# Kernel optimization log

Hardware: AMD Instinct MI355X
Metric: run time of the kernel (lower is better)

## Reference

```python
import jax, jax.numpy as jnp
import numpy as np

S = 3072        # total tokens (3 images x 1024 patches)
E = 1280        # n_embed
H = 16          # n_heads
HD = E // H     # head_dim = 80
NSEG = 3


def rotate_half(x):
    x1 = x[..., : x.shape[-1] // 2]
    x2 = x[..., x.shape[-1] // 2 :]
    return jnp.concatenate((-x2, x1), axis=-1)


def setup_inputs() -> dict:
    key = jax.random.key(0)
    ks = jax.random.split(key, 6)
    x = jax.random.normal(ks[0], (S, E), dtype=jnp.float32)
    rotary_pos_emb = jax.random.normal(ks[1], (S, HD // 2), dtype=jnp.float32)
    qkv_w = jax.random.normal(ks[2], (3 * E, E), dtype=jnp.float32) * 0.02
    qkv_b = jax.random.normal(ks[3], (3 * E,), dtype=jnp.float32) * 0.02
    proj_w = jax.random.normal(ks[4], (E, E), dtype=jnp.float32) * 0.02
    proj_b = jax.random.normal(ks[5], (E,), dtype=jnp.float32) * 0.02
    cu_seqlens = (jnp.arange(NSEG + 1, dtype=jnp.int32) * (S // NSEG))  # [0,1024,2048,3072]
    return {"x": x, "rotary_pos_emb": rotary_pos_emb, "qkv_w": qkv_w,
            "qkv_b": qkv_b, "proj_w": proj_w, "proj_b": proj_b,
            "cu_seqlens": cu_seqlens}


def reference(x, rotary_pos_emb, qkv_w, qkv_b, proj_w, proj_b, cu_seqlens):
    seq_len = x.shape[0]
    # qkv projection (torch Linear: x @ W.T + b)
    qkv = (x @ qkv_w.T + qkv_b).reshape(seq_len, 3, H, HD)
    q, k, v = qkv[:, 0], qkv[:, 1], qkv[:, 2]          # each [S, H, HD]

    # inline RoPE: cos/sin repeated over the two halves of head_dim
    cos = jnp.cos(rotary_pos_emb)
    sin = jnp.sin(rotary_pos_emb)
    cos = jnp.concatenate([cos, cos], axis=-1)[:, None, :]  # [S, 1, HD]
    sin = jnp.concatenate([sin, sin], axis=-1)[:, None, :]
    q = q * cos + rotate_half(q) * sin
    k = k * cos + rotate_half(k) * sin

    # block-diagonal segment mask from cu_seqlens
    seg = jnp.searchsorted(cu_seqlens, jnp.arange(seq_len), side="right")  # [S]
    mask = seg[:, None] == seg[None, :]                 # [S, S] bool

    scale = jnp.asarray(1.0 / np.sqrt(HD), dtype=q.dtype)
    scores = jnp.einsum("qhd,khd->hqk", q, k) * scale   # [H, S, S]
    scores = jnp.where(mask[None], scores, jnp.finfo(scores.dtype).min)
    attn = jax.nn.softmax(scores, axis=-1)
    out = jnp.einsum("hqk,khd->qhd", attn, v).reshape(seq_len, E)
    return out @ proj_w.T + proj_b
```

## Files before the change

kernel.cpp:

```cpp
#include <hip/hip_runtime.h>
#include <hip/hip_bf16.h>
#include <math.h>

#define SEQ   3072
#define EMB   1280
#define NHEAD 16
#define HDIM  80
#define QKVN  3840
#define NSEGS 3

typedef __attribute__((ext_vector_type(8))) short bf16x8;
typedef __attribute__((ext_vector_type(4))) short bf16x4;
typedef __attribute__((ext_vector_type(4))) float f32x4;

__device__ __forceinline__ short f2bf(float f) {
    __hip_bfloat16 h = __float2bfloat16(f);
    return *reinterpret_cast<short*>(&h);
}
__device__ __forceinline__ float bf2f(short s) {
    unsigned int u = ((unsigned int)(unsigned short)s) << 16;
    union { unsigned int u; float f; } c; c.u = u;
    return c.f;
}

__device__ __forceinline__ void gload_lds16(const void* g, void* l) {
    __builtin_amdgcn_global_load_lds(
        (const __attribute__((address_space(1))) unsigned int*)g,
        (__attribute__((address_space(3))) unsigned int*)l, 16, 0, 0);
}

__global__ __launch_bounds__(256)
void cvt3_kernel(const float* __restrict__ a, short* __restrict__ oa, int na8,
                 const float* __restrict__ b, short* __restrict__ ob, int nb8,
                 const float* __restrict__ c, short* __restrict__ oc, int nc8)
{
    int j = blockIdx.x * 256 + threadIdx.x;
    const float* src; short* dst;
    if (j < na8) { src = a; dst = oa; }
    else if ((j -= na8) < nb8) { src = b; dst = ob; }
    else { j -= nb8; src = c; dst = oc; }
    float4 x = *reinterpret_cast<const float4*>(&src[j*8]);
    float4 y = *reinterpret_cast<const float4*>(&src[j*8+4]);
    bf16x8 o;
    o[0]=f2bf(x.x); o[1]=f2bf(x.y); o[2]=f2bf(x.z); o[3]=f2bf(x.w);
    o[4]=f2bf(y.x); o[5]=f2bf(y.y); o[6]=f2bf(y.z); o[7]=f2bf(y.w);
    *reinterpret_cast<bf16x8*>(&dst[j*8]) = o;
}

__device__ __forceinline__ void store_val(float v, float* p) { *p = v; }
__device__ __forceinline__ void store_val(float v, short* p) { *p = f2bf(v); }

template<typename OT, bool SWZ>
__global__ __launch_bounds__(256)
void gemm_bf16_nt(const short* __restrict__ A, int lda,
                  const short* __restrict__ B,
                  const float* __restrict__ bias, OT* __restrict__ C,
                  int M, int N, int K)
{
    __shared__ short As[128][32];
    __shared__ short Bs[128][32];

    int bx, by;
    if (SWZ) {
        const int flat = blockIdx.x;
        const int xcd  = flat & 7;
        const int i    = flat >> 3;
        by = xcd * 3 + (i % 3);
        bx = i / 3;
    } else {
        bx = blockIdx.x;
        by = blockIdx.y;
    }

    const int tid = threadIdx.x;
    const int w   = tid >> 6;
    const int l   = tid & 63;
    const int l15 = l & 15;
    const int l4  = l >> 4;
    const int wr  = w >> 1;
    const int wc  = w & 1;
    const int row0 = by * 128;
    const int col0 = bx * 128;

    const int srow = l >> 2;
    const int sk   = (l & 3) * 8;

    f32x4 acc[4][4];
    #pragma unroll
    for (int mi = 0; mi < 4; ++mi)
        #pragma unroll
        for (int ni = 0; ni < 4; ++ni) acc[mi][ni] = (f32x4){0.f,0.f,0.f,0.f};

    for (int k0 = 0; k0 < K; k0 += 32) {
        {
            const int c0 = w, c1 = w + 4;
            gload_lds16(&A[(size_t)(row0 + c0*16 + srow) * lda + k0 + sk], &As[c0*16][0]);
            gload_lds16(&A[(size_t)(row0 + c1*16 + srow) * lda + k0 + sk], &As[c1*16][0]);
            gload_lds16(&B[(size_t)(col0 + c0*16 + srow) * K   + k0 + sk], &Bs[c0*16][0]);
            gload_lds16(&B[(size_t)(col0 + c1*16 + srow) * K   + k0 + sk], &Bs[c1*16][0]);
        }
        __syncthreads();

        bf16x8 af[4], bfr[4];
        #pragma unroll
        for (int mi = 0; mi < 4; ++mi)
            af[mi] = *reinterpret_cast<const bf16x8*>(&As[wr*64 + mi*16 + l15][l4*8]);
        #pragma unroll
        for (int ni = 0; ni < 4; ++ni)
            bfr[ni] = *reinterpret_cast<const bf16x8*>(&Bs[wc*64 + ni*16 + l15][l4*8]);

        #pragma unroll
        for (int mi = 0; mi < 4; ++mi)
            #pragma unroll
            for (int ni = 0; ni < 4; ++ni)
                acc[mi][ni] = __builtin_amdgcn_mfma_f32_16x16x32_bf16(
                    af[mi], bfr[ni], acc[mi][ni], 0, 0, 0);
        __syncthreads();
    }

    #pragma unroll
    for (int ni = 0; ni < 4; ++ni) {
        int col = col0 + wc*64 + ni*16 + l15;
        float bv = bias[col];
        #pragma unroll
        for (int mi = 0; mi < 4; ++mi) {
            #pragma unroll
            for (int r = 0; r < 4; ++r) {
                size_t row = (size_t)(row0 + wr*64 + mi*16 + l4*4 + r);
                store_val(acc[mi][ni][r] + bv, &C[row * (size_t)N + col]);
            }
        }
    }
}

template<typename OT>
__global__ __launch_bounds__(256)
void gemm_bf16_nt64(const short* __restrict__ A, int lda,
                    const short* __restrict__ B,
                    const float* __restrict__ bias, OT* __restrict__ C,
                    int M, int N, int K)
{
    __shared__ short As[128][32];
    __shared__ short Bs[64][32];

    const int tid = threadIdx.x;
    const int w   = tid >> 6;
    const int l   = tid & 63;
    const int l15 = l & 15;
    const int l4  = l >> 4;
    const int wr  = w >> 1;
    const int wc  = w & 1;
    const int row0 = blockIdx.y * 128;
    const int col0 = blockIdx.x * 64;

    const int srow = l >> 2;
    const int sk   = (l & 3) * 8;

    f32x4 acc[4][2];
    #pragma unroll
    for (int mi = 0; mi < 4; ++mi)
        #pragma unroll
        for (int ni = 0; ni < 2; ++ni) acc[mi][ni] = (f32x4){0.f,0.f,0.f,0.f};

    for (int k0 = 0; k0 < K; k0 += 32) {
        {
            const int c0 = w, c1 = w + 4;
            gload_lds16(&A[(size_t)(row0 + c0*16 + srow) * lda + k0 + sk], &As[c0*16][0]);
            gload_lds16(&A[(size_t)(row0 + c1*16 + srow) * lda + k0 + sk], &As[c1*16][0]);
            gload_lds16(&B[(size_t)(col0 + w*16  + srow) * K   + k0 + sk], &Bs[w*16][0]);
        }
        __syncthreads();

        bf16x8 af[4], bfr[2];
        #pragma unroll
        for (int mi = 0; mi < 4; ++mi)
            af[mi] = *reinterpret_cast<const bf16x8*>(&As[wr*64 + mi*16 + l15][l4*8]);
        #pragma unroll
        for (int ni = 0; ni < 2; ++ni)
            bfr[ni] = *reinterpret_cast<const bf16x8*>(&Bs[wc*32 + ni*16 + l15][l4*8]);

        #pragma unroll
        for (int mi = 0; mi < 4; ++mi)
            #pragma unroll
            for (int ni = 0; ni < 2; ++ni)
                acc[mi][ni] = __builtin_amdgcn_mfma_f32_16x16x32_bf16(
                    af[mi], bfr[ni], acc[mi][ni], 0, 0, 0);
        __syncthreads();
    }

    #pragma unroll
    for (int ni = 0; ni < 2; ++ni) {
        int col = col0 + wc*32 + ni*16 + l15;
        float bv = bias[col];
        #pragma unroll
        for (int mi = 0; mi < 4; ++mi) {
            #pragma unroll
            for (int r = 0; r < 4; ++r) {
                size_t row = (size_t)(row0 + wr*64 + mi*16 + l4*4 + r);
                store_val(acc[mi][ni][r] + bv, &C[row * (size_t)N + col]);
            }
        }
    }
}

__global__ __launch_bounds__(256)
void rope_bf16_kernel(short* __restrict__ qkv, const float* __restrict__ rpe)
{
    int idx = blockIdx.x * 256 + threadIdx.x;
    int blk = idx % 5;
    int h   = (idx / 5) % NHEAD;
    int s   = (idx / (5*NHEAD)) % SEQ;
    int t   = idx / (5*NHEAD*SEQ);
    int d0  = blk * 8;

    const float* rp = rpe + s*40 + d0;
    short* p = qkv + (size_t)s*QKVN + t*EMB + h*HDIM + d0;
    bf16x8 v0 = *reinterpret_cast<const bf16x8*>(p);
    bf16x8 v1 = *reinterpret_cast<const bf16x8*>(p + 40);
    bf16x8 o0, o1;
    #pragma unroll
    for (int j = 0; j < 8; ++j) {
        float ang = rp[j];
        float sn = sinf(ang), cs = cosf(ang);
        float a = bf2f(v0[j]), b = bf2f(v1[j]);
        o0[j] = f2bf(a*cs - b*sn);
        o1[j] = f2bf(b*cs + a*sn);
    }
    *reinterpret_cast<bf16x8*>(p)      = o0;
    *reinterpret_cast<bf16x8*>(p + 40) = o1;
}

__global__ __launch_bounds__(256, 4)
void attn_mfma(const short* __restrict__ qkv, const int* __restrict__ cu,
               short* __restrict__ aout)
{
    const int flat = blockIdx.x;
    const int xcd  = flat & 7;
    const int rem  = flat >> 3;
    const int qt   = rem & 15;
    const int shhi = rem >> 4;
    const int sh   = xcd + 8*shhi;
    const int h    = sh / 3;
    const int seg  = sh - 3*h;
    const int s0 = cu[seg], s1 = cu[seg+1];

    const int tid = threadIdx.x;
    const int w   = tid >> 6;
    const int l   = tid & 63;
    const int l15 = l & 15;
    const int l4  = l >> 4;

    __shared__ short Kl[64][128];
    __shared__ short Vt[HDIM][64];

    const int q0 = s0 + qt*64 + w*16;

    bf16x8 bzero;
    #pragma unroll
    for (int j = 0; j < 8; ++j) bzero[j] = 0;

    bf16x8 qf[3];
    {
        const short* qp = qkv + (size_t)(q0 + l15) * QKVN + h*HDIM;
        qf[0] = *reinterpret_cast<const bf16x8*>(qp + l4*8);
        qf[1] = *reinterpret_cast<const bf16x8*>(qp + 32 + l4*8);
        qf[2] = (l4 < 2) ? *reinterpret_cast<const bf16x8*>(qp + 64 + l4*8) : bzero;
    }

    float m = -3.4e38f, lsum = 0.f;
    f32x4 O[5];
    #pragma unroll
    for (int dt = 0; dt < 5; ++dt) O[dt] = (f32x4){0.f,0.f,0.f,0.f};

    int kkey[3], ku[3];
    const short* kptr[3];
    short* klds[3];
    #pragma unroll
    for (int i = 0; i < 3; ++i) {
        int task = tid + i*256;
        kkey[i] = task / 12;
        ku[i]   = task - kkey[i]*12;
        kptr[i] = qkv + (size_t)(s0 + kkey[i])*QKVN + EMB + h*HDIM + ku[i]*8;
        klds[i] = &Kl[kkey[i]][(ku[i] ^ (kkey[i] & 7))*8];
    }

    const int vu  = ((l >> 2) & 3) | ((l >> 5) << 2);
    const int vbs = ((l >> 4) & 1) * 4 + (l & 3);
    const int vd0 = w * 20;
    const short* vp1 = qkv + (size_t)(s0 + l) * QKVN + 2*EMB + h*HDIM + vd0;

    bf16x8 kreg[3];
    bf16x8 vA, vB;
    bf16x4 vC;
    #pragma unroll
    for (int i = 0; i < 3; ++i)
        kreg[i] = (ku[i] < 10) ? *reinterpret_cast<const bf16x8*>(kptr[i]) : bzero;
    vA = *reinterpret_cast<const bf16x8*>(vp1);
    vB = *reinterpret_cast<const bf16x8*>(vp1 + 8);
    vC = *reinterpret_cast<const bf16x4*>(vp1 + 16);

    const float scale2 = 0.1612982054f;
    const int nk = s1 - s0;
    const size_t step = (size_t)64 * QKVN;
    short* vt_flat = &Vt[0][0];

    for (int kc = 0; kc < nk; kc += 64) {
        __syncthreads();

        #pragma unroll
        for (int i = 0; i < 3; ++i)
            *reinterpret_cast<bf16x8*>(klds[i]) = kreg[i];
        #pragma unroll
        for (int e = 0; e < 8; ++e) {
            int d = vd0 + e;
            vt_flat[d*64 + ((vu ^ (d & 7)) & 7)*8 + vbs] = vA[e];
        }
        #pragma unroll
        for (int e = 0; e < 8; ++e) {
            int d = vd0 + 8 + e;
            vt_flat[d*64 + ((vu ^ (d & 7)) & 7)*8 + vbs] = vB[e];
        }
        #pragma unroll
        for (int e = 0; e < 4; ++e) {
            int d = vd0 + 16 + e;
            vt_flat[d*64 + ((vu ^ (d & 7)) & 7)*8 + vbs] = vC[e];
        }

        if (kc + 64 < nk) {
            #pragma unroll
            for (int i = 0; i < 3; ++i) {
                kptr[i] += step;
                if (ku[i] < 10) kreg[i] = *reinterpret_cast<const bf16x8*>(kptr[i]);
            }
            vp1 += step;
            vA = *reinterpret_cast<const bf16x8*>(vp1);
            vB = *reinterpret_cast<const bf16x8*>(vp1 + 8);
            vC = *reinterpret_cast<const bf16x4*>(vp1 + 16);
        }
        __syncthreads();

        f32x4 S[4];
        __builtin_amdgcn_s_setprio(1);
        #pragma unroll
        for (int ct = 0; ct < 4; ++ct) {
            f32x4 acc = (f32x4){0.f,0.f,0.f,0.f};
            int key = ct*16 + l15;
            #pragma unroll
            for (int t = 0; t < 3; ++t) {
                int u = (4*t + l4) ^ (key & 7);
                bf16x8 a = *reinterpret_cast<const bf16x8*>(&Kl[key][u*8]);
                acc = __builtin_amdgcn_mfma_f32_16x16x32_bf16(a, qf[t], acc, 0, 0, 0);
            }
            S[ct] = acc;
        }
        __builtin_amdgcn_s_setprio(0);

        float mxr = -3.4e38f;
        #pragma unroll
        for (int ct = 0; ct < 4; ++ct)
            #pragma unroll
            for (int r = 0; r < 4; ++r) mxr = fmaxf(mxr, S[ct][r]);
        float mx = mxr * scale2;
        mx = fmaxf(mx, __shfl_xor(mx, 16));
        mx = fmaxf(mx, __shfl_xor(mx, 32));
        if (!__all(mx - m <= 8.f)) {
            float mn   = fmaxf(m, mx);
            float corr = exp2f(m - mn);
            lsum *= corr;
            #pragma unroll
            for (int dt = 0; dt < 5; ++dt)
                #pragma unroll
                for (int r = 0; r < 4; ++r) O[dt][r] *= corr;
            m = mn;
        }
        float p[4][4];
        float ps = 0.f;
        #pragma unroll
        for (int ct = 0; ct < 4; ++ct)
            #pragma unroll
            for (int r = 0; r < 4; ++r) {
                float e = exp2f(fmaf(S[ct][r], scale2, -m));
                p[ct][r] = e;
                ps += e;
            }
        ps += __shfl_xor(ps, 16);
        ps += __shfl_xor(ps, 32);
        lsum += ps;

        #pragma unroll
        for (int s2 = 0; s2 < 2; ++s2) {
            bf16x8 pb;
            #pragma unroll
            for (int j = 0; j < 8; ++j)
                pb[j] = f2bf(p[2*s2 + (j>>2)][j & 3]);
            __builtin_amdgcn_s_setprio(1);
            #pragma unroll
            for (int dt = 0; dt < 5; ++dt) {
                int d = dt*16 + l15;
                bf16x8 va = *reinterpret_cast<const bf16x8*>(
                    &vt_flat[d*64 + (((4*s2 + l4) ^ (d & 7)) & 7)*8]);
                O[dt] = __builtin_amdgcn_mfma_f32_16x16x32_bf16(va, pb, O[dt], 0, 0, 0);
            }
            __builtin_amdgcn_s_setprio(0);
        }
    }

    float inv = 1.f / lsum;
    short* orow = aout + (size_t)(q0 + l15) * EMB + h*HDIM;
    #pragma unroll
    for (int dt = 0; dt < 5; ++dt) {
        bf16x4 o4;
        #pragma unroll
        for (int r = 0; r < 4; ++r) o4[r] = f2bf(O[dt][r] * inv);
        *reinterpret_cast<bf16x4*>(&orow[dt*16 + 4*l4]) = o4;
    }
}

extern "C" void kernel_launch(void* const* d_in, const int* in_sizes, int n_in,
                              void* d_out, int out_size, void* d_ws, size_t ws_size,
                              hipStream_t stream)
{
    const float* x      = (const float*)d_in[0];
    const float* rpe    = (const float*)d_in[1];
    const float* qkv_w  = (const float*)d_in[2];
    const float* qkv_b  = (const float*)d_in[3];
    const float* proj_w = (const float*)d_in[4];
    const float* proj_b = (const float*)d_in[5];
    const int*   cu     = (const int*)d_in[6];
    float* out = (float*)d_out;

    short* ws       = (short*)d_ws;
    short* qkv_bf   = ws;
    short* x_bf     = qkv_bf  + (size_t)SEQ * QKVN;
    short* qkvw_bf  = x_bf    + (size_t)SEQ * EMB;
    short* projw_bf = qkvw_bf + (size_t)QKVN * EMB;
    short* attn_bf  = projw_bf+ (size_t)EMB * EMB;

    dim3 blk(256);

    const int na8 = SEQ*EMB/8, nb8 = QKVN*EMB/8, nc8 = EMB*EMB/8;
    cvt3_kernel<<<dim3((na8+nb8+nc8)/256), blk, 0, stream>>>(
        x, x_bf, na8, qkv_w, qkvw_bf, nb8, proj_w, projw_bf, nc8);

    gemm_bf16_nt<short, true><<<dim3((QKVN/128)*(SEQ/128)), blk, 0, stream>>>(
        x_bf, EMB, qkvw_bf, qkv_b, qkv_bf, SEQ, QKVN, EMB);

    rope_bf16_kernel<<<dim3(2*SEQ*NHEAD*5/256), blk, 0, stream>>>(qkv_bf, rpe);

    attn_mfma<<<dim3(16*NSEGS*NHEAD), blk, 0, stream>>>(qkv_bf, cu, attn_bf);

    gemm_bf16_nt64<float><<<dim3(EMB/64, SEQ/128), blk, 0, stream>>>(
        attn_bf, EMB, projw_bf, proj_b, out, SEQ, EMB, EMB);
}
```

Before: 136.2 us.

## Double-buffer LDS tiles in bf16 GEMM kernels to overlap loads with MFMA

Both NT GEMM kernels now use two LDS buffers for A and B tiles, issuing the async global-to-LDS load for the next K-slice before computing on the current one. This cuts barriers per K step from two to one and hides global load latency behind MFMA work. It doubles LDS usage per block, which may reduce occupancy.

```diff
diff --git a/kernel.cpp b/kernel.cpp
--- a/kernel.cpp
+++ b/kernel.cpp
@@ -57,8 +57,8 @@
                   const float* __restrict__ bias, OT* __restrict__ C,
                   int M, int N, int K)
 {
-    __shared__ short As[128][32];
-    __shared__ short Bs[128][32];
+    __shared__ short As0[128][32], Bs0[128][32];
+    __shared__ short As1[128][32], Bs1[128][32];
 
     int bx, by;
     if (SWZ) {
@@ -84,6 +84,7 @@
 
     const int srow = l >> 2;
     const int sk   = (l & 3) * 8;
+    const int c0 = w, c1 = w + 4;
 
     f32x4 acc[4][4];
     #pragma unroll
@@ -91,32 +92,44 @@
         #pragma unroll
         for (int ni = 0; ni < 4; ++ni) acc[mi][ni] = (f32x4){0.f,0.f,0.f,0.f};
 
-    for (int k0 = 0; k0 < K; k0 += 32) {
-        {
-            const int c0 = w, c1 = w + 4;
-            gload_lds16(&A[(size_t)(row0 + c0*16 + srow) * lda + k0 + sk], &As[c0*16][0]);
-            gload_lds16(&A[(size_t)(row0 + c1*16 + srow) * lda + k0 + sk], &As[c1*16][0]);
-            gload_lds16(&B[(size_t)(col0 + c0*16 + srow) * K   + k0 + sk], &Bs[c0*16][0]);
-            gload_lds16(&B[(size_t)(col0 + c1*16 + srow) * K   + k0 + sk], &Bs[c1*16][0]);
-        }
-        __syncthreads();
-
-        bf16x8 af[4], bfr[4];
-        #pragma unroll
-        for (int mi = 0; mi < 4; ++mi)
-            af[mi] = *reinterpret_cast<const bf16x8*>(&As[wr*64 + mi*16 + l15][l4*8]);
-        #pragma unroll
-        for (int ni = 0; ni < 4; ++ni)
-            bfr[ni] = *reinterpret_cast<const bf16x8*>(&Bs[wc*64 + ni*16 + l15][l4*8]);
-
-        #pragma unroll
-        for (int mi = 0; mi < 4; ++mi)
-            #pragma unroll
-            for (int ni = 0; ni < 4; ++ni)
-                acc[mi][ni] = __builtin_amdgcn_mfma_f32_16x16x32_bf16(
-                    af[mi], bfr[ni], acc[mi][ni], 0, 0, 0);
-        __syncthreads();
-    }
+#define STAGE_NT(AS, BS, KOFF)                                                          \
+    do {                                                                                \
+        gload_lds16(&A[(size_t)(row0 + c0*16 + srow) * lda + (KOFF) + sk], &AS[c0*16][0]); \
+        gload_lds16(&A[(size_t)(row0 + c1*16 + srow) * lda + (KOFF) + sk], &AS[c1*16][0]); \
+        gload_lds16(&B[(size_t)(col0 + c0*16 + srow) * K   + (KOFF) + sk], &BS[c0*16][0]); \
+        gload_lds16(&B[(size_t)(col0 + c1*16 + srow) * K   + (KOFF) + sk], &BS[c1*16][0]); \
+    } while (0)
+
+#define COMPUTE_NT(AS, BS)                                                              \
+    do {                                                                                \
+        bf16x8 af[4], bfr[4];                                                           \
+        _Pragma("unroll")                                                               \
+        for (int mi = 0; mi < 4; ++mi)                                                  \
+            af[mi] = *reinterpret_cast<const bf16x8*>(&AS[wr*64 + mi*16 + l15][l4*8]);  \
+        _Pragma("unroll")                                                               \
+        for (int ni = 0; ni < 4; ++ni)                                                  \
+            bfr[ni] = *reinterpret_cast<const bf16x8*>(&BS[wc*64 + ni*16 + l15][l4*8]); \
+        _Pragma("unroll")                                                               \
+        for (int mi = 0; mi < 4; ++mi)                                                  \
+            _Pragma("unroll")                                                           \
+            for (int ni = 0; ni < 4; ++ni)                                              \
+                acc[mi][ni] = __builtin_amdgcn_mfma_f32_16x16x32_bf16(                  \
+                    af[mi], bfr[ni], acc[mi][ni], 0, 0, 0);                             \
+    } while (0)
+
+    STAGE_NT(As0, Bs0, 0);
+    __syncthreads();
+
+    for (int k0 = 0; k0 < K; k0 += 64) {
+        if (k0 + 32 < K) STAGE_NT(As1, Bs1, k0 + 32);
+        COMPUTE_NT(As0, Bs0);
+        __syncthreads();
+        if (k0 + 64 < K) STAGE_NT(As0, Bs0, k0 + 64);
+        COMPUTE_NT(As1, Bs1);
+        __syncthreads();
+    }
+#undef STAGE_NT
+#undef COMPUTE_NT
 
     #pragma unroll
     for (int ni = 0; ni < 4; ++ni) {
@@ -140,8 +153,8 @@
                     const float* __restrict__ bias, OT* __restrict__ C,
                     int M, int N, int K)
 {
-    __shared__ short As[128][32];
-    __shared__ short Bs[64][32];
+    __shared__ short As0[128][32], Bs0[64][32];
+    __shared__ short As1[128][32], Bs1[64][32];
 
     const int tid = threadIdx.x;
     const int w   = tid >> 6;
@@ -155,6 +168,7 @@
 
     const int srow = l >> 2;
     const int sk   = (l & 3) * 8;
+    const int c0 = w, c1 = w + 4;
 
     f32x4 acc[4][2];
     #pragma unroll
@@ -162,31 +176,43 @@
         #pragma unroll
         for (int ni = 0; ni < 2; ++ni) acc[mi][ni] = (f32x4){0.f,0.f,0.f,0.f};
 
-    for (int k0 = 0; k0 < K; k0 += 32) {
-        {
-            const int c0 = w, c1 = w + 4;
-            gload_lds16(&A[(size_t)(row0 + c0*16 + srow) * lda + k0 + sk], &As[c0*16][0]);
-            gload_lds16(&A[(size_t)(row0 + c1*16 + srow) * lda + k0 + sk], &As[c1*16][0]);
-            gload_lds16(&B[(size_t)(col0 + w*16  + srow) * K   + k0 + sk], &Bs[w*16][0]);
-        }
-        __syncthreads();
-
-        bf16x8 af[4], bfr[2];
-        #pragma unroll
-        for (int mi = 0; mi < 4; ++mi)
-            af[mi] = *reinterpret_cast<const bf16x8*>(&As[wr*64 + mi*16 + l15][l4*8]);
-        #pragma unroll
-        for (int ni = 0; ni < 2; ++ni)
-            bfr[ni] = *reinterpret_cast<const bf16x8*>(&Bs[wc*32 + ni*16 + l15][l4*8]);
-
-        #pragma unroll
-        for (int mi = 0; mi < 4; ++mi)
-            #pragma unroll
-            for (int ni = 0; ni < 2; ++ni)
-                acc[mi][ni] = __builtin_amdgcn_mfma_f32_16x16x32_bf16(
-                    af[mi], bfr[ni], acc[mi][ni], 0, 0, 0);
-        __syncthreads();
-    }
+#define STAGE_NT64(AS, BS, KOFF)                                                        \
+    do {                                                                                \
+        gload_lds16(&A[(size_t)(row0 + c0*16 + srow) * lda + (KOFF) + sk], &AS[c0*16][0]); \
+        gload_lds16(&A[(size_t)(row0 + c1*16 + srow) * lda + (KOFF) + sk], &AS[c1*16][0]); \
+        gload_lds16(&B[(size_t)(col0 + w*16  + srow) * K   + (KOFF) + sk], &BS[w*16][0]);  \
+    } while (0)
+
+#define COMPUTE_NT64(AS, BS)                                                            \
+    do {                                                                                \
+        bf16x8 af[4], bfr[2];                                                           \
+        _Pragma("unroll")                                                               \
+        for (int mi = 0; mi < 4; ++mi)                                                  \
+            af[mi] = *reinterpret_cast<const bf16x8*>(&AS[wr*64 + mi*16 + l15][l4*8]);  \
+        _Pragma("unroll")                                                               \
+        for (int ni = 0; ni < 2; ++ni)                                                  \
+            bfr[ni] = *reinterpret_cast<const bf16x8*>(&BS[wc*32 + ni*16 + l15][l4*8]); \
+        _Pragma("unroll")                                                               \
+        for (int mi = 0; mi < 4; ++mi)                                                  \
+            _Pragma("unroll")                                                           \
+            for (int ni = 0; ni < 2; ++ni)                                              \
+                acc[mi][ni] = __builtin_amdgcn_mfma_f32_16x16x32_bf16(                  \
+                    af[mi], bfr[ni], acc[mi][ni], 0, 0, 0);                             \
+    } while (0)
+
+    STAGE_NT64(As0, Bs0, 0);
+    __syncthreads();
+
+    for (int k0 = 0; k0 < K; k0 += 64) {
+        if (k0 + 32 < K) STAGE_NT64(As1, Bs1, k0 + 32);
+        COMPUTE_NT64(As0, Bs0);
+        __syncthreads();
+        if (k0 + 64 < K) STAGE_NT64(As0, Bs0, k0 + 64);
+        COMPUTE_NT64(As1, Bs1);
+        __syncthreads();
+    }
+#undef STAGE_NT64
+#undef COMPUTE_NT64
 
     #pragma unroll
     for (int ni = 0; ni < 2; ++ni) {
```

Result: faster. 128.9 us (-5.4%).
